# Kernel optimization log

Hardware: AMD Instinct MI355X
Metric: run time of the kernel (lower is better)

The kernel has to match this reference:

```python
import jax, jax.numpy as jnp
import numpy as np

B, T, F, H, FC = 32, 2048, 128, 512, 128


def setup_inputs() -> dict:
    key = jax.random.key(0)
    ks = jax.random.split(key, 10)
    x = jax.random.normal(ks[0], (B, T, F), dtype=jnp.float32)
    lengths = jax.random.randint(ks[1], (B,), 1, T + 1)
    s = 1.0 / np.sqrt(H)  # torch nn.RNN init: U(-1/sqrt(hidden), 1/sqrt(hidden))
    W_ih = jax.random.uniform(ks[2], (H, F), jnp.float32, -s, s)
    W_hh = jax.random.uniform(ks[3], (H, H), jnp.float32, -s, s)
    b_ih = jax.random.uniform(ks[4], (H,), jnp.float32, -s, s)
    b_hh = jax.random.uniform(ks[5], (H,), jnp.float32, -s, s)
    s1 = 1.0 / np.sqrt(H)
    W1 = jax.random.uniform(ks[6], (FC, H), jnp.float32, -s1, s1)
    b1 = jax.random.uniform(ks[7], (FC,), jnp.float32, -s1, s1)
    s2 = 1.0 / np.sqrt(FC)
    W2 = jax.random.uniform(ks[8], (1, FC), jnp.float32, -s2, s2)
    b2 = jax.random.uniform(ks[9], (1,), jnp.float32, -s2, s2)
    return {"x": x, "lengths": lengths, "W_ih": W_ih, "W_hh": W_hh,
            "b_ih": b_ih, "b_hh": b_hh, "W1": W1, "b1": b1, "W2": W2, "b2": b2}


def reference(x, lengths, W_ih, W_hh, b_ih, b_hh, W1, b1, W2, b2):
    # x: [B, T, F] padded ragged sequences; lengths: [B]
    Bs, Ts, Fs = x.shape
    Hs = W_ih.shape[0]
    mask = jnp.arange(Ts)[None, :] < lengths[:, None]          # [B, T]
    xs = (jnp.swapaxes(x, 0, 1), mask.T)                       # time-major [T, B, ...]

    def step(h, inp):
        x_t, m_t = inp
        # vanilla RNN cell: h' = tanh(W_ih x + b_ih + W_hh h + b_hh)
        h_new = jnp.tanh(x_t @ W_ih.T + b_ih + h @ W_hh.T + b_hh)
        h = jnp.where(m_t[:, None], h_new, h)                  # freeze hidden past seq end
        return h, h_new

    h0 = jnp.zeros((Bs, Hs), dtype=x.dtype)
    h_final, outp = jax.lax.scan(step, h0, xs)                 # h_final [B,H], outp [T,B,H]

    # fcn: Linear(H,128) -> Linear(128,1) -> ReLU, applied to every timestep output
    n = jax.nn.relu((outp @ W1.T + b1) @ W2.T + b2)            # [T, B, 1]
    pos = (n[..., 0] > 0) & mask.T                             # count only valid timesteps
    outs = jnp.sum(pos, axis=0).astype(jnp.float32)[:, None]   # [B, 1]
    return outs, h_final
```

## Files before the change

kernel.cpp:

```cpp
#include <hip/hip_runtime.h>
#include <math.h>
#include <stdint.h>

#define BB 32
#define TT 2048
#define FF 128
#define HH 512
#define FCC 128
#define QW 8
#define NTH 640

#define SCALE_F     4194304.0f
#define INV_SCALE_F (1.0f/4194304.0f)
#define CNT_ONE     (1ull<<48)
#define BIAS_TOTAL  (1ll<<46)
#define BIAS_SHARE  (1ll<<43)

#define WS_U64 (2*BB*HH + BB*16*8 + BB)

typedef float f32x2 __attribute__((ext_vector_type(2)));

__global__ void ws_zero(uint64_t* g) {
    size_t i = (size_t)blockIdx.x * blockDim.x + threadIdx.x;
    if (i < WS_U64) g[i] = 0ull;
}

__device__ __forceinline__ void wait_lgkm0() {
    asm volatile("s_waitcnt lgkmcnt(0)" ::: "memory");
}

__device__ __forceinline__ float fast_tanh(float z) {
    float ax = fabsf(z);
    float e  = __expf(-2.0f * ax);
    float r  = (1.0f - e) / (1.0f + e);
    return copysignf(r, z);
}

__device__ __forceinline__ void pk_fma(f32x2& d, f32x2 a, f32x2 b) {
    asm("v_pk_fma_f32 %0, %1, %2, %0" : "+v"(d) : "v"(a), "v"(b));
}
__device__ __forceinline__ f32x2 lo2(float4 v) { f32x2 r; r.x = v.x; r.y = v.y; return r; }
__device__ __forceinline__ f32x2 hi2(float4 v) { f32x2 r; r.x = v.z; r.y = v.w; return r; }

__device__ __forceinline__ uint64_t gld_agent(const uint64_t* p) {
    return __hip_atomic_load(p, __ATOMIC_RELAXED, __HIP_MEMORY_SCOPE_AGENT);
}
__device__ __forceinline__ int flag_ld(const int* p) {
    return __hip_atomic_load(p, __ATOMIC_RELAXED, __HIP_MEMORY_SCOPE_WORKGROUP);
}

__global__ __launch_bounds__(NTH, 1)
void rnn_seq(const float* __restrict__ x, const int* __restrict__ lengths,
             const float* __restrict__ W_ih, const float* __restrict__ W_hh,
             const float* __restrict__ b_ih, const float* __restrict__ b_hh,
             const float* __restrict__ W1, const float* __restrict__ b1,
             const float* __restrict__ W2, const float* __restrict__ b2,
             float* __restrict__ out, uint64_t* __restrict__ ws)
{
    const int blk  = blockIdx.x;
    const int b    = blk & 31;
    const int q    = blk >> 5;
    const int tid  = threadIdx.x;
    const int w    = tid >> 6;
    const int lane = tid & 63;
    const int len  = lengths[b];

    uint64_t* gh  = ws;
    uint64_t* gsd = ws + 2 * BB * HH;
    uint64_t* gx  = gsd + BB * 16 * 8;

    __shared__ float hsh[2][64];
    __shared__ float biass[64];
    __shared__ int   flag_s;
    __shared__ int   lok_s;

    if (w == 8) {
        biass[lane] = b_ih[q * 64 + lane] + b_hh[q * 64 + lane];
        hsh[0][lane] = 0.0f;
        uint32_t xcc_raw;
        asm volatile("s_getreg_b32 %0, hwreg(HW_REG_XCC_ID)" : "=s"(xcc_raw));
        const uint32_t xcc = xcc_raw & 7;
        if (lane == 0) {
            flag_s = 0;
            uint64_t* gxp = gx + b;
            __hip_atomic_fetch_add(gxp, 1ull << (8 * xcc),
                                   __ATOMIC_RELAXED, __HIP_MEMORY_SCOPE_AGENT);
            uint64_t v;
            do { v = gld_agent(gxp); }
            while ((uint8_t)((v * 0x0101010101010101ull) >> 56) != 8);
            lok_s = (v == (8ull << (8 * xcc))) ? 1 : 0;
        }
    }
    __syncthreads();
    const bool lok = (lok_s != 0);

    if (w < 8) {
        const int r = w * 64 + lane;
        float4 ww[16];
        { const float4* p = (const float4*)(W_hh + (size_t)r * HH + q * 64);
          #pragma unroll
          for (int k = 0; k < 16; ++k) ww[k] = p[k]; }
        float4 wi[4];
        { const float4* p = (const float4*)(W_ih + r * FF + q * 16);
          #pragma unroll
          for (int k = 0; k < 4; ++k) wi[k] = p[k]; }
        float wvreg = 0.0f;
        if (w == 7) {
            const int col = q * 64 + lane;
            #pragma unroll 8
            for (int f = 0; f < FCC; ++f) wvreg += W2[f] * W1[f * HH + col];
        }
        int prevI[2] = {0, 0};
        const float* xb = x + (size_t)b * TT * FF + q * 16;
        float4 xc[4], xn[4];
        { const float4* p = (const float4*)xb;
          #pragma unroll
          for (int k = 0; k < 4; ++k) xc[k] = p[k]; }
        { const float4* p = (const float4*)(xb + FF);
          #pragma unroll
          for (int k = 0; k < 4; ++k) xn[k] = p[k]; }

        uint64_t* ghb = gh + (size_t)b * HH + r;

        for (int i = 0; i < len; ++i) {
            f32x2 acc01 = {0.0f, 0.0f};
            f32x2 acc23 = {0.0f, 0.0f};
            #pragma unroll
            for (int k = 0; k < 4; ++k) {
                pk_fma(acc01, lo2(wi[k]), lo2(xc[k]));
                pk_fma(acc23, hi2(wi[k]), hi2(xc[k]));
            }

            while (flag_ld(&flag_s) < i) {}
            const float* hc = hsh[i & 1];
            const float4* hq = (const float4*)hc;
            #pragma unroll
            for (int k = 0; k < 16; ++k) {
                float4 hk = hq[k];
                pk_fma(acc01, lo2(ww[k]), lo2(hk));
                pk_fma(acc23, hi2(ww[k]), hi2(hk));
            }
            float A = (acc01.x + acc01.y) + (acc23.x + acc23.y);

            float hown = 0.0f;
            if (w == 7) hown = hc[lane];

            int fi = __float2int_rn(A * SCALE_F);
            const int pn = (i + 1) & 1;
            long long con = (long long)CNT_ONE + (long long)(fi - prevI[pn])
                          + ((i < 2) ? BIAS_SHARE : 0);
            prevI[pn] = fi;
            uint64_t* slot = ghb + (size_t)pn * BB * HH;
            if (lok)
                __hip_atomic_fetch_add(slot, (uint64_t)con,
                                       __ATOMIC_RELAXED, __HIP_MEMORY_SCOPE_WORKGROUP);
            else
                atomicAdd((unsigned long long*)slot, (unsigned long long)con);

            if (w == 7 && i > 0) {
                float d = hown * wvreg;
                d += __shfl_xor(d, 1);  d += __shfl_xor(d, 2);
                d += __shfl_xor(d, 4);  d += __shfl_xor(d, 8);
                d += __shfl_xor(d, 16); d += __shfl_xor(d, 32);
                if (lane == 0) {
                    uint64_t pk = ((uint64_t)(uint32_t)i << 32) |
                                  (uint64_t)__float_as_uint(d);
                    __hip_atomic_store(&gsd[((size_t)b * 16 + (i & 15)) * 8 + q],
                                       pk, __ATOMIC_RELAXED, __HIP_MEMORY_SCOPE_AGENT);
                }
            }
            #pragma unroll
            for (int k = 0; k < 4; ++k) xc[k] = xn[k];
            if (i + 2 < len) {
                const float4* p = (const float4*)(xb + (size_t)(i + 2) * FF);
                #pragma unroll
                for (int k = 0; k < 4; ++k) xn[k] = p[k];
            }
        }
        if (w == 7) {
            while (flag_ld(&flag_s) < len) {}
            float d = hsh[len & 1][lane] * wvreg;
            d += __shfl_xor(d, 1);  d += __shfl_xor(d, 2);
            d += __shfl_xor(d, 4);  d += __shfl_xor(d, 8);
            d += __shfl_xor(d, 16); d += __shfl_xor(d, 32);
            if (lane == 0) {
                uint64_t pk = ((uint64_t)(uint32_t)len << 32) |
                              (uint64_t)__float_as_uint(d);
                __hip_atomic_store(&gsd[((size_t)b * 16 + (len & 15)) * 8 + q],
                                   pk, __ATOMIC_RELAXED, __HIP_MEMORY_SCOPE_AGENT);
            }
        }
    } else if (w == 8) {
        __builtin_amdgcn_s_setprio(1);
        uint64_t z = 0;
        asm("" : "+v"(z));
        float hval = 0.0f;
        for (int i = 0; i < len; ++i) {
            const int j  = i + 1;
            const int pn = j & 1;
            const uint64_t target = 8ull * (uint64_t)((j + 1) >> 1);
            uint64_t* pr = gh + (size_t)pn * BB * HH + (size_t)b * HH + q * 64 + lane;
            uint64_t u;
            if (lok) {
                do { u = __hip_atomic_fetch_add(pr, z, __ATOMIC_RELAXED,
                                                __HIP_MEMORY_SCOPE_WORKGROUP); }
                while ((u >> 48) != target);
            } else {
                do { u = gld_agent(pr); } while ((u >> 48) != target);
            }
            float pre = (float)(int)(uint32_t)u * INV_SCALE_F + biass[lane];
            hval = fast_tanh(pre);
            hsh[pn][lane] = hval;
            wait_lgkm0();
            if (lane == 0)
                __hip_atomic_store(&flag_s, j, __ATOMIC_RELAXED,
                                   __HIP_MEMORY_SCOPE_WORKGROUP);
        }
        out[BB + b * HH + q * 64 + lane] = hval;
    } else {
        if (q != 0) return;
        float cconst = b2[0];
        for (int f = 0; f < FCC; ++f) cconst += W2[f] * b1[f];
        int count = 0;
        for (int j = 1; j <= len; ++j) {
            float d = 0.0f;
            if (lane < 8) {
                uint64_t* pr = gsd + ((size_t)b * 16 + (j & 15)) * 8 + lane;
                uint64_t u;
                do { u = gld_agent(pr); }
                while ((int)(u >> 32) != j);
                d = __uint_as_float((uint32_t)u);
            }
            d += __shfl_xor(d, 1); d += __shfl_xor(d, 2); d += __shfl_xor(d, 4);
            if (lane == 0 && d + cconst > 0.0f) ++count;
        }
        if (lane == 0) out[b] = (float)count;
    }
}

extern "C" void kernel_launch(void* const* d_in, const int* in_sizes, int n_in,
                              void* d_out, int out_size, void* d_ws, size_t ws_size,
                              hipStream_t stream) {
    const float* x    = (const float*)d_in[0];
    const int*   lens = (const int*)d_in[1];
    const float* W_ih = (const float*)d_in[2];
    const float* W_hh = (const float*)d_in[3];
    const float* b_ih = (const float*)d_in[4];
    const float* b_hh = (const float*)d_in[5];
    const float* W1   = (const float*)d_in[6];
    const float* b1   = (const float*)d_in[7];
    const float* W2   = (const float*)d_in[8];
    const float* b2   = (const float*)d_in[9];
    float* out = (float*)d_out;
    uint64_t* ws = (uint64_t*)d_ws;

    ws_zero<<<dim3(145), dim3(256), 0, stream>>>(ws);
    rnn_seq<<<dim3(BB * QW), dim3(NTH), 0, stream>>>(
        x, lens, W_ih, W_hh, b_ih, b_hh, W1, b1, W2, b2, out, ws);
}
```

Before: 2.767 ms.

## Replace LDS flag spin-wait with hardware workgroup barriers per timestep

Replaces the shared-memory flag that compute waves polled each step with s_barrier calls that all ten waves in the block execute once per timestep. The input projection for the next step is computed before the barrier so it overlaps the wait. The count wave is restructured to poll gsd non-blockingly inside the barrier loop and drain any remaining steps afterward. Idle waves in non-q0 blocks now also loop on barriers. The aim is to cut LDS polling traffic and wake-up latency, at the risk of coupling every wave to the slowest one each step.

After: 2.666 ms. -3.6%, faster.

```diff
diff --git a/kernel.cpp b/kernel.cpp
--- a/kernel.cpp
+++ b/kernel.cpp
@@ -29,6 +29,12 @@
     asm volatile("s_waitcnt lgkmcnt(0)" ::: "memory");
 }
 
+__device__ __forceinline__ void wg_barrier() {
+    asm volatile("" ::: "memory");
+    __builtin_amdgcn_s_barrier();
+    asm volatile("" ::: "memory");
+}
+
 __device__ __forceinline__ float fast_tanh(float z) {
     float ax = fabsf(z);
     float e  = __expf(-2.0f * ax);
@@ -44,9 +50,6 @@
 
 __device__ __forceinline__ uint64_t gld_agent(const uint64_t* p) {
     return __hip_atomic_load(p, __ATOMIC_RELAXED, __HIP_MEMORY_SCOPE_AGENT);
-}
-__device__ __forceinline__ int flag_ld(const int* p) {
-    return __hip_atomic_load(p, __ATOMIC_RELAXED, __HIP_MEMORY_SCOPE_WORKGROUP);
 }
 
 __global__ __launch_bounds__(NTH, 1)
@@ -71,7 +74,6 @@
 
     __shared__ float hsh[2][64];
     __shared__ float biass[64];
-    __shared__ int   flag_s;
     __shared__ int   lok_s;
 
     if (w == 8) {
@@ -81,7 +83,6 @@
         asm volatile("s_getreg_b32 %0, hwreg(HW_REG_XCC_ID)" : "=s"(xcc_raw));
         const uint32_t xcc = xcc_raw & 7;
         if (lane == 0) {
-            flag_s = 0;
             uint64_t* gxp = gx + b;
             __hip_atomic_fetch_add(gxp, 1ull << (8 * xcc),
                                    __ATOMIC_RELAXED, __HIP_MEMORY_SCOPE_AGENT);
@@ -122,16 +123,15 @@
 
         uint64_t* ghb = gh + (size_t)b * HH + r;
 
+        f32x2 acc01 = {0.0f, 0.0f};
+        f32x2 acc23 = {0.0f, 0.0f};
+        #pragma unroll
+        for (int k = 0; k < 4; ++k) {
+            pk_fma(acc01, lo2(wi[k]), lo2(xc[k]));
+            pk_fma(acc23, hi2(wi[k]), hi2(xc[k]));
+        }
+
         for (int i = 0; i < len; ++i) {
-            f32x2 acc01 = {0.0f, 0.0f};
-            f32x2 acc23 = {0.0f, 0.0f};
-            #pragma unroll
-            for (int k = 0; k < 4; ++k) {
-                pk_fma(acc01, lo2(wi[k]), lo2(xc[k]));
-                pk_fma(acc23, hi2(wi[k]), hi2(xc[k]));
-            }
-
-            while (flag_ld(&flag_s) < i) {}
             const float* hc = hsh[i & 1];
             const float4* hq = (const float4*)hc;
             #pragma unroll
@@ -176,9 +176,16 @@
                 #pragma unroll
                 for (int k = 0; k < 4; ++k) xn[k] = p[k];
             }
+            acc01.x = 0.0f; acc01.y = 0.0f;
+            acc23.x = 0.0f; acc23.y = 0.0f;
+            #pragma unroll
+            for (int k = 0; k < 4; ++k) {
+                pk_fma(acc01, lo2(wi[k]), lo2(xc[k]));
+                pk_fma(acc23, hi2(wi[k]), hi2(xc[k]));
+            }
+            wg_barrier();
         }
         if (w == 7) {
-            while (flag_ld(&flag_s) < len) {}
             float d = hsh[len & 1][lane] * wvreg;
             d += __shfl_xor(d, 1);  d += __shfl_xor(d, 2);
             d += __shfl_xor(d, 4);  d += __shfl_xor(d, 8);
@@ -212,29 +219,43 @@
             hval = fast_tanh(pre);
             hsh[pn][lane] = hval;
             wait_lgkm0();
-            if (lane == 0)
-                __hip_atomic_store(&flag_s, j, __ATOMIC_RELAXED,
-                                   __HIP_MEMORY_SCOPE_WORKGROUP);
+            wg_barrier();
         }
         out[BB + b * HH + q * 64 + lane] = hval;
-    } else {
-        if (q != 0) return;
+    } else if (q == 0) {
         float cconst = b2[0];
         for (int f = 0; f < FCC; ++f) cconst += W2[f] * b1[f];
         int count = 0;
-        for (int j = 1; j <= len; ++j) {
+        int jn = 1;
+        uint64_t upend = 0;
+        for (int i = 0; i < len; ++i) {
+            bool ok = (lane < 8) ? ((int)(upend >> 32) == jn) : true;
+            if (__all(ok)) {
+                float d = (lane < 8) ? __uint_as_float((uint32_t)upend) : 0.0f;
+                d += __shfl_xor(d, 1); d += __shfl_xor(d, 2); d += __shfl_xor(d, 4);
+                if (lane == 0 && d + cconst > 0.0f) ++count;
+                ++jn;
+            }
+            upend = (lane < 8)
+                  ? gld_agent(gsd + ((size_t)b * 16 + (jn & 15)) * 8 + lane)
+                  : 0ull;
+            wg_barrier();
+        }
+        while (jn <= len) {
             float d = 0.0f;
             if (lane < 8) {
-                uint64_t* pr = gsd + ((size_t)b * 16 + (j & 15)) * 8 + lane;
+                uint64_t* pr = gsd + ((size_t)b * 16 + (jn & 15)) * 8 + lane;
                 uint64_t u;
-                do { u = gld_agent(pr); }
-                while ((int)(u >> 32) != j);
+                do { u = gld_agent(pr); } while ((int)(u >> 32) != jn);
                 d = __uint_as_float((uint32_t)u);
             }
             d += __shfl_xor(d, 1); d += __shfl_xor(d, 2); d += __shfl_xor(d, 4);
             if (lane == 0 && d + cconst > 0.0f) ++count;
+            ++jn;
         }
         if (lane == 0) out[b] = (float)count;
+    } else {
+        for (int i = 0; i < len; ++i) wg_barrier();
     }
 }
 
```
